# Optimization experiments

Hardware: AMD Instinct MI355X
Metric: run time of the kernel (lower is better)

## Reference

```python
import jax, jax.numpy as jnp
import numpy as np

XI = 4.0  # init kwarg


def _gaussian_kernel(xi: float):
    radius = int(3 * xi)
    coords = jnp.arange(-radius, radius + 1, dtype=jnp.float32)
    g1 = jnp.exp(-coords ** 2 / (2 * xi * xi))
    g1 = g1 / g1.sum()
    # dense 3D outer-product kernel, shape (K, K, K)
    g3 = g1[:, None, None] * g1[None, :, None] * g1[None, None, :]
    K = g3.shape[0]
    # grouped depthwise weight: (out=3, in/groups=1, K, K, K)
    return jnp.broadcast_to(g3[None, None], (3, 1, K, K, K))


def setup_inputs() -> dict:
    key = jax.random.key(0)
    x = jax.random.normal(key, (1, 3, 160, 160, 160), dtype=jnp.float32)
    kernel = _gaussian_kernel(XI)
    return {"x": x, "kernel": kernel}


def reference(x, kernel):
    # grouped Conv3d, groups=3 (depthwise), 'same' padding of radius each side
    r = (kernel.shape[-1] - 1) // 2
    return jax.lax.conv_general_dilated(
        x, kernel,
        window_strides=(1, 1, 1),
        padding=[(r, r), (r, r), (r, r)],
        dimension_numbers=("NCDHW", "OIDHW", "NCDHW"),
        feature_group_count=3,
    )
```

## Files before the change

### kernel.cpp

```cpp
#include <hip/hip_runtime.h>
#include <hip/hip_fp16.h>


#define NV 160
constexpr int KS    = 25;
constexpr int RAD   = 12;
constexpr int PLANE = NV * NV;
constexpr int VOL   = NV * NV * NV;
constexpr int TOT   = 3 * VOL;
constexpr int ROWS  = NV + 2 * RAD;

constexpr int PITCH = 17;
constexpr int OPT   = 10;
constexpr int WIN   = OPT + KS - 1;
constexpr int OROW  = 168;

constexpr int QP    = 9;
constexpr int OPT4  = 5;
constexpr int WIN4  = OPT4 + KS - 1;

__device__ __forceinline__ void pk(float2& a, float2 g, float2 v) {
    asm("v_pk_fma_f32 %0, %1, %2, %0" : "+v"(a) : "v"(g), "v"(v));
}

__device__ __forceinline__ void load_g(const float* __restrict__ k3, float* g) {
    float c   = k3[12 * 625 + 312];
    float g12 = cbrtf(c);
    float inv = 1.0f / (g12 * g12);
#pragma unroll
    for (int t = 0; t < KS; ++t) g[t] = k3[t * 625 + 312] * inv;
}

__device__ __forceinline__ void unpack8(uint4 raw, float4& lo, float4& hi) {
    __half2* hp = (__half2*)&raw;
    float2 a = __half22float2(hp[0]);
    float2 b = __half22float2(hp[1]);
    float2 c = __half22float2(hp[2]);
    float2 d = __half22float2(hp[3]);
    lo = make_float4(a.x, a.y, b.x, b.y);
    hi = make_float4(c.x, c.y, d.x, d.y);
}

__global__ __launch_bounds__(256) void conv_w(const float* __restrict__ in,
                                              __half* __restrict__ out,
                                              const float* __restrict__ k3) {
    __shared__ float2 T[ROWS][PITCH];
    float gs[KS];
    load_g(k3, gs);
    float2 g2[KS];
#pragma unroll
    for (int t = 0; t < KS; ++t) g2[t] = make_float2(gs[t], gs[t]);

    int tid = threadIdx.x;
    int b   = blockIdx.x;
    int ht  = b % 5;
    int cd  = b / 5;
    int h0  = ht * 32;
    const float* base = in + (size_t)cd * PLANE;

    int wl = tid & 31, hq = tid >> 5;
#pragma unroll
    for (int hh = 0; hh < 2; ++hh) {
        int hp = hq + hh * 8;
        const float* r0 = base + (h0 + 2 * hp) * NV;
#pragma unroll
        for (int ib = 0; ib < ROWS; ib += 32) {
            int i = ib + wl;
            if (i < ROWS) {
                int wv = i - RAD;
                float a = 0.f, bb = 0.f;
                if (wv >= 0 && wv < NV) { a = r0[wv]; bb = r0[NV + wv]; }
                T[i][hp] = make_float2(a, bb);
            }
        }
    }
    __syncthreads();

    int p  = tid & 15;
    int ct = tid >> 4;
    int wb = ct * OPT;
    float2 acc[OPT];
#pragma unroll
    for (int j = 0; j < OPT; ++j) acc[j] = make_float2(0.f, 0.f);
#pragma unroll
    for (int it = 0; it < WIN; ++it) {
        float2 v = T[wb + it][p];
#pragma unroll
        for (int j = 0; j < OPT; ++j) {
            int t = it - j;
            if (t >= 0 && t < KS) pk(acc[j], g2[t], v);
        }
    }

    __syncthreads();
    __half* Ost = (__half*)(&T[0][0]);
#pragma unroll
    for (int j = 0; j < OPT; ++j) {
        Ost[(2 * p)     * OROW + wb + j] = __float2half_rn(acc[j].x);
        Ost[(2 * p + 1) * OROW + wb + j] = __float2half_rn(acc[j].y);
    }
    __syncthreads();
    __half* ob = out + (size_t)cd * PLANE + (size_t)h0 * NV;
#pragma unroll
    for (int it = 0; it < 3; ++it) {
        int task = it * 256 + tid;
        if (task < 640) {
            int chunk = task % 20, row = task / 20;
            uint4 v = *(const uint4*)(Ost + row * OROW + 8 * chunk);
            *(uint4*)(ob + (size_t)row * NV + 8 * chunk) = v;
        }
    }
}

__global__ __launch_bounds__(256) void conv_h(const __half* __restrict__ in,
                                              __half* __restrict__ out,
                                              const float* __restrict__ k3) {
    __shared__ float4 T4[ROWS][QP];
    float gs[KS];
    load_g(k3, gs);
    float2 g2[KS];
#pragma unroll
    for (int t = 0; t < KS; ++t) g2[t] = make_float2(gs[t], gs[t]);

    int tid = threadIdx.x;
    int b   = blockIdx.x;
    int wt  = b % 5;
    int cd  = b / 5;
    int w0  = wt * 32;
    const __half* base = in + (size_t)cd * PLANE + w0;

    int e = tid & 3, r0 = tid >> 2;
#pragma unroll
    for (int ib = 0; ib < ROWS; ib += 64) {
        int i = ib + r0;
        if (i < ROWS) {
            int h = i - RAD;
            float4 lo = make_float4(0.f, 0.f, 0.f, 0.f), hi = lo;
            if (h >= 0 && h < NV) {
                uint4 raw = *(const uint4*)(base + h * NV + 8 * e);
                unpack8(raw, lo, hi);
            }
            T4[i][2 * e]     = lo;
            T4[i][2 * e + 1] = hi;
        }
    }
    __syncthreads();

    int wq = tid & 7, ct = tid >> 3;
    int hb = ct * OPT4;
    float2 alo[OPT4], ahi[OPT4];
#pragma unroll
    for (int j = 0; j < OPT4; ++j) { alo[j] = make_float2(0.f, 0.f); ahi[j] = alo[j]; }
#pragma unroll
    for (int it = 0; it < WIN4; ++it) {
        float4 v = T4[hb + it][wq];
        float2 vlo = make_float2(v.x, v.y);
        float2 vhi = make_float2(v.z, v.w);
#pragma unroll
        for (int j = 0; j < OPT4; ++j) {
            int t = it - j;
            if (t >= 0 && t < KS) { pk(alo[j], g2[t], vlo); pk(ahi[j], g2[t], vhi); }
        }
    }
    __half* ob = out + (size_t)cd * PLANE + w0 + 4 * wq;
#pragma unroll
    for (int j = 0; j < OPT4; ++j) {
        __half2 o01 = __float22half2_rn(make_float2(alo[j].x, alo[j].y));
        __half2 o23 = __float22half2_rn(make_float2(ahi[j].x, ahi[j].y));
        __half* pdst = ob + (hb + j) * NV;
        *(__half2*)(pdst)     = o01;
        *(__half2*)(pdst + 2) = o23;
    }
}

__global__ __launch_bounds__(256) void conv_d(const __half* __restrict__ in,
                                              float* __restrict__ out,
                                              const float* __restrict__ k3) {
    __shared__ float4 T4[ROWS][QP];
    float gs[KS];
    load_g(k3, gs);
    float2 g2[KS];
#pragma unroll
    for (int t = 0; t < KS; ++t) g2[t] = make_float2(gs[t], gs[t]);

    int tid = threadIdx.x;
    int b   = blockIdx.x;
    int wt  = b % 5;
    int ch  = b / 5;
    int c   = ch / NV, h = ch % NV;
    int w0  = wt * 32;
    const __half* base = in + (size_t)c * VOL + h * NV + w0;

    int e = tid & 3, r0 = tid >> 2;
#pragma unroll
    for (int ib = 0; ib < ROWS; ib += 64) {
        int i = ib + r0;
        if (i < ROWS) {
            int d = i - RAD;
            float4 lo = make_float4(0.f, 0.f, 0.f, 0.f), hi = lo;
            if (d >= 0 && d < NV) {
                uint4 raw = *(const uint4*)(base + (size_t)d * PLANE + 8 * e);
                unpack8(raw, lo, hi);
            }
            T4[i][2 * e]     = lo;
            T4[i][2 * e + 1] = hi;
        }
    }
    __syncthreads();

    int wq = tid & 7, ct = tid >> 3;
    int db = ct * OPT4;
    float2 alo[OPT4], ahi[OPT4];
#pragma unroll
    for (int j = 0; j < OPT4; ++j) { alo[j] = make_float2(0.f, 0.f); ahi[j] = alo[j]; }
#pragma unroll
    for (int it = 0; it < WIN4; ++it) {
        float4 v = T4[db + it][wq];
        float2 vlo = make_float2(v.x, v.y);
        float2 vhi = make_float2(v.z, v.w);
#pragma unroll
        for (int j = 0; j < OPT4; ++j) {
            int t = it - j;
            if (t >= 0 && t < KS) { pk(alo[j], g2[t], vlo); pk(ahi[j], g2[t], vhi); }
        }
    }
    float* ob = out + (size_t)c * VOL + h * NV + w0 + 4 * wq;
#pragma unroll
    for (int j = 0; j < OPT4; ++j)
        *(float4*)(ob + (size_t)(db + j) * PLANE) =
            make_float4(alo[j].x, alo[j].y, ahi[j].x, ahi[j].y);
}

__global__ __launch_bounds__(256) void conv3d_direct(const float* __restrict__ x,
                                                     const float* __restrict__ k3,
                                                     float* __restrict__ out) {
    int idx = blockIdx.x * 256 + threadIdx.x;
    if (idx >= TOT) return;
    int w = idx % NV;
    int t = idx / NV;
    int h = t % NV; t /= NV;
    int d = t % NV;
    int c = t / NV;
    const float* kc = k3 + c * (KS * KS * KS);
    float acc = 0.f;
    for (int i = 0; i < KS; ++i) {
        int dd = d + i - RAD;
        if (dd < 0 || dd >= NV) continue;
        for (int j = 0; j < KS; ++j) {
            int hh = h + j - RAD;
            if (hh < 0 || hh >= NV) continue;
            const float* xr = x + (c * NV + dd) * NV * NV + hh * NV + (w - RAD);
            const float* kr = kc + (i * KS + j) * KS;
            int k0 = (RAD - w) > 0 ? (RAD - w) : 0;
            int k1 = (NV + RAD - w) < KS ? (NV + RAD - w) : KS;
            for (int k = k0; k < k1; ++k) acc += kr[k] * xr[k];
        }
    }
    out[idx] = acc;
}

extern "C" void kernel_launch(void* const* d_in, const int* in_sizes, int n_in,
                              void* d_out, int out_size, void* d_ws, size_t ws_size,
                              hipStream_t stream) {
    const float* x  = (const float*)d_in[0];
    const float* k3 = (const float*)d_in[1];
    float* out = (float*)d_out;

    if (ws_size >= (size_t)TOT * 2 * sizeof(__half)) {
        __half* tmpA = (__half*)d_ws;
        __half* tmpB = tmpA + TOT;
        conv_w<<<2400, 256, 0, stream>>>(x, tmpA, k3);
        conv_h<<<2400, 256, 0, stream>>>(tmpA, tmpB, k3);
        conv_d<<<2400, 256, 0, stream>>>(tmpB, out, k3);
    } else {
        conv3d_direct<<<(TOT + 255) / 256, 256, 0, stream>>>(x, k3, out);
    }
}
```

Measured before the change: 57.03 us.

## Retile H and D passes to full-width 80-row tiles with half2 shared storage

The H and D separable passes now each give a block the full 160-wide row and half of the axis (80 outputs plus a 24-row halo), instead of 32-wide column strips covering the whole axis. Tiles stay in fp16 (half2) in shared memory and are converted at read time rather than unpacked to fp32 on load, which halves the LDS footprint. Each of the 320 threads computes two groups of 10 outputs for one half2 column pair. The block count drops to 960, and the halo is reloaded per half, so each input row is fetched more often.

Measured after the change: 55.34 us. 3.0% less time.

```diff
diff --git a/kernel.cpp b/kernel.cpp
--- a/kernel.cpp
+++ b/kernel.cpp
@@ -15,9 +15,10 @@
 constexpr int WIN   = OPT + KS - 1;
 constexpr int OROW  = 168;
 
-constexpr int QP    = 9;
-constexpr int OPT4  = 5;
-constexpr int WIN4  = OPT4 + KS - 1;
+constexpr int HC2   = 80;
+constexpr int TR    = HC2 + 2 * RAD;
+constexpr int TP2   = 84;
+constexpr int NTASK = TR * 20;
 
 __device__ __forceinline__ void pk(float2& a, float2 g, float2 v) {
     asm("v_pk_fma_f32 %0, %1, %2, %0" : "+v"(a) : "v"(g), "v"(v));
@@ -29,16 +30,6 @@
     float inv = 1.0f / (g12 * g12);
 #pragma unroll
     for (int t = 0; t < KS; ++t) g[t] = k3[t * 625 + 312] * inv;
-}
-
-__device__ __forceinline__ void unpack8(uint4 raw, float4& lo, float4& hi) {
-    __half2* hp = (__half2*)&raw;
-    float2 a = __half22float2(hp[0]);
-    float2 b = __half22float2(hp[1]);
-    float2 c = __half22float2(hp[2]);
-    float2 d = __half22float2(hp[3]);
-    lo = make_float4(a.x, a.y, b.x, b.y);
-    hi = make_float4(c.x, c.y, d.x, d.y);
 }
 
 __global__ __launch_bounds__(256) void conv_w(const float* __restrict__ in,
@@ -112,10 +103,10 @@
     }
 }
 
-__global__ __launch_bounds__(256) void conv_h(const __half* __restrict__ in,
+__global__ __launch_bounds__(320) void conv_h(const __half* __restrict__ in,
                                               __half* __restrict__ out,
                                               const float* __restrict__ k3) {
-    __shared__ float4 T4[ROWS][QP];
+    __shared__ __half2 T[TR][TP2];
     float gs[KS];
     load_g(k3, gs);
     float2 g2[KS];
@@ -124,59 +115,52 @@
 
     int tid = threadIdx.x;
     int b   = blockIdx.x;
-    int wt  = b % 5;
-    int cd  = b / 5;
-    int w0  = wt * 32;
-    const __half* base = in + (size_t)cd * PLANE + w0;
-
-    int e = tid & 3, r0 = tid >> 2;
-#pragma unroll
-    for (int ib = 0; ib < ROWS; ib += 64) {
-        int i = ib + r0;
-        if (i < ROWS) {
-            int h = i - RAD;
-            float4 lo = make_float4(0.f, 0.f, 0.f, 0.f), hi = lo;
-            if (h >= 0 && h < NV) {
-                uint4 raw = *(const uint4*)(base + h * NV + 8 * e);
-                unpack8(raw, lo, hi);
+    int hh  = b & 1;
+    int cd  = b >> 1;
+    int h0  = hh * HC2;
+    const __half* base = in + (size_t)cd * PLANE;
+
+#pragma unroll
+    for (int it = 0; it < 7; ++it) {
+        int task = it * 320 + tid;
+        if (task < NTASK) {
+            int r = task / 20, k = task % 20;
+            int hg = h0 - RAD + r;
+            uint4 v = make_uint4(0u, 0u, 0u, 0u);
+            if (hg >= 0 && hg < NV)
+                v = *(const uint4*)(base + hg * NV + 8 * k);
+            *(uint4*)(&T[r][4 * k]) = v;
+        }
+    }
+    __syncthreads();
+
+    int wp = tid % 80, oc = tid / 80;
+#pragma unroll
+    for (int hv = 0; hv < 2; ++hv) {
+        int rb = (oc + 4 * hv) * OPT;
+        float2 acc[OPT];
+#pragma unroll
+        for (int j = 0; j < OPT; ++j) acc[j] = make_float2(0.f, 0.f);
+#pragma unroll
+        for (int it = 0; it < WIN; ++it) {
+            float2 v = __half22float2(T[rb + it][wp]);
+#pragma unroll
+            for (int j = 0; j < OPT; ++j) {
+                int t = it - j;
+                if (t >= 0 && t < KS) pk(acc[j], g2[t], v);
             }
-            T4[i][2 * e]     = lo;
-            T4[i][2 * e + 1] = hi;
-        }
-    }
-    __syncthreads();
-
-    int wq = tid & 7, ct = tid >> 3;
-    int hb = ct * OPT4;
-    float2 alo[OPT4], ahi[OPT4];
-#pragma unroll
-    for (int j = 0; j < OPT4; ++j) { alo[j] = make_float2(0.f, 0.f); ahi[j] = alo[j]; }
-#pragma unroll
-    for (int it = 0; it < WIN4; ++it) {
-        float4 v = T4[hb + it][wq];
-        float2 vlo = make_float2(v.x, v.y);
-        float2 vhi = make_float2(v.z, v.w);
-#pragma unroll
-        for (int j = 0; j < OPT4; ++j) {
-            int t = it - j;
-            if (t >= 0 && t < KS) { pk(alo[j], g2[t], vlo); pk(ahi[j], g2[t], vhi); }
-        }
-    }
-    __half* ob = out + (size_t)cd * PLANE + w0 + 4 * wq;
-#pragma unroll
-    for (int j = 0; j < OPT4; ++j) {
-        __half2 o01 = __float22half2_rn(make_float2(alo[j].x, alo[j].y));
-        __half2 o23 = __float22half2_rn(make_float2(ahi[j].x, ahi[j].y));
-        __half* pdst = ob + (hb + j) * NV;
-        *(__half2*)(pdst)     = o01;
-        *(__half2*)(pdst + 2) = o23;
-    }
-}
-
-__global__ __launch_bounds__(256) void conv_d(const __half* __restrict__ in,
+        }
+        __half* op = out + (size_t)cd * PLANE + (size_t)(h0 + rb) * NV + 2 * wp;
+#pragma unroll
+        for (int j = 0; j < OPT; ++j)
+            *(__half2*)(op + j * NV) = __float22half2_rn(acc[j]);
+    }
+}
+
+__global__ __launch_bounds__(320) void conv_d(const __half* __restrict__ in,
                                               float* __restrict__ out,
                                               const float* __restrict__ k3) {
-    __shared__ float4 T4[ROWS][QP];
+    __shared__ __half2 T[TR][TP2];
     float gs[KS];
     load_g(k3, gs);
     float2 g2[KS];
@@ -185,50 +169,47 @@
 
     int tid = threadIdx.x;
     int b   = blockIdx.x;
-    int wt  = b % 5;
-    int ch  = b / 5;
+    int dh  = b & 1;
+    int ch  = b >> 1;
     int c   = ch / NV, h = ch % NV;
-    int w0  = wt * 32;
-    const __half* base = in + (size_t)c * VOL + h * NV + w0;
-
-    int e = tid & 3, r0 = tid >> 2;
-#pragma unroll
-    for (int ib = 0; ib < ROWS; ib += 64) {
-        int i = ib + r0;
-        if (i < ROWS) {
-            int d = i - RAD;
-            float4 lo = make_float4(0.f, 0.f, 0.f, 0.f), hi = lo;
-            if (d >= 0 && d < NV) {
-                uint4 raw = *(const uint4*)(base + (size_t)d * PLANE + 8 * e);
-                unpack8(raw, lo, hi);
+    int d0  = dh * HC2;
+    const __half* base = in + (size_t)c * VOL + h * NV;
+
+#pragma unroll
+    for (int it = 0; it < 7; ++it) {
+        int task = it * 320 + tid;
+        if (task < NTASK) {
+            int r = task / 20, k = task % 20;
+            int dg = d0 - RAD + r;
+            uint4 v = make_uint4(0u, 0u, 0u, 0u);
+            if (dg >= 0 && dg < NV)
+                v = *(const uint4*)(base + (size_t)dg * PLANE + 8 * k);
+            *(uint4*)(&T[r][4 * k]) = v;
+        }
+    }
+    __syncthreads();
+
+    int wp = tid % 80, oc = tid / 80;
+#pragma unroll
+    for (int hv = 0; hv < 2; ++hv) {
+        int rb = (oc + 4 * hv) * OPT;
+        float2 acc[OPT];
+#pragma unroll
+        for (int j = 0; j < OPT; ++j) acc[j] = make_float2(0.f, 0.f);
+#pragma unroll
+        for (int it = 0; it < WIN; ++it) {
+            float2 v = __half22float2(T[rb + it][wp]);
+#pragma unroll
+            for (int j = 0; j < OPT; ++j) {
+                int t = it - j;
+                if (t >= 0 && t < KS) pk(acc[j], g2[t], v);
             }
-            T4[i][2 * e]     = lo;
-            T4[i][2 * e + 1] = hi;
-        }
-    }
-    __syncthreads();
-
-    int wq = tid & 7, ct = tid >> 3;
-    int db = ct * OPT4;
-    float2 alo[OPT4], ahi[OPT4];
-#pragma unroll
-    for (int j = 0; j < OPT4; ++j) { alo[j] = make_float2(0.f, 0.f); ahi[j] = alo[j]; }
-#pragma unroll
-    for (int it = 0; it < WIN4; ++it) {
-        float4 v = T4[db + it][wq];
-        float2 vlo = make_float2(v.x, v.y);
-        float2 vhi = make_float2(v.z, v.w);
-#pragma unroll
-        for (int j = 0; j < OPT4; ++j) {
-            int t = it - j;
-            if (t >= 0 && t < KS) { pk(alo[j], g2[t], vlo); pk(ahi[j], g2[t], vhi); }
-        }
-    }
-    float* ob = out + (size_t)c * VOL + h * NV + w0 + 4 * wq;
-#pragma unroll
-    for (int j = 0; j < OPT4; ++j)
-        *(float4*)(ob + (size_t)(db + j) * PLANE) =
-            make_float4(alo[j].x, alo[j].y, ahi[j].x, ahi[j].y);
+        }
+        float* op = out + (size_t)c * VOL + h * NV + 2 * wp;
+#pragma unroll
+        for (int j = 0; j < OPT; ++j)
+            *(float2*)(op + (size_t)(d0 + rb + j) * PLANE) = acc[j];
+    }
 }
 
 __global__ __launch_bounds__(256) void conv3d_direct(const float* __restrict__ x,
@@ -270,8 +251,8 @@
         __half* tmpA = (__half*)d_ws;
         __half* tmpB = tmpA + TOT;
         conv_w<<<2400, 256, 0, stream>>>(x, tmpA, k3);
-        conv_h<<<2400, 256, 0, stream>>>(tmpA, tmpB, k3);
-        conv_d<<<2400, 256, 0, stream>>>(tmpB, out, k3);
+        conv_h<<<480 * 2, 320, 0, stream>>>(tmpA, tmpB, k3);
+        conv_d<<<480 * 2, 320, 0, stream>>>(tmpB, out, k3);
     } else {
         conv3d_direct<<<(TOT + 255) / 256, 256, 0, stream>>>(x, k3, out);
     }
```
